# Kernel tuning notes

Measured on AMD Instinct MI355X. Metric: run time of the kernel, lower is better.

The kernel has to match this reference:

```python
import jax, jax.numpy as jnp
import numpy as np

N = 32768          # total nodes
B = 64             # number of graphs (batch.max()+1)
IN_C = 256
OUT_C = 256
NUM_SCALES = 4
NUM_HEADS = 8
BN_EPS = 1e-5


def setup_inputs() -> dict:
    key = jax.random.key(0)
    ks = jax.random.split(key, 10)
    out_s = OUT_C // NUM_SCALES
    x = jax.random.normal(ks[0], (N, IN_C), jnp.float32)
    spectral = jax.random.normal(ks[1], (NUM_SCALES, N, IN_C), jnp.float32)
    batch = jnp.sort(jax.random.randint(ks[2], (N,), 0, B)).astype(jnp.int64)
    # per-scale Linear weights (glorot) and zero biases; stored as [S, in, out_s]
    g = (6.0 / (IN_C + out_s)) ** 0.5
    Ws = jax.random.uniform(ks[3], (NUM_SCALES, IN_C, out_s), jnp.float32, -g, g)
    bs = jnp.zeros((NUM_SCALES, out_s), jnp.float32)
    # MultiheadAttention params (torch layout: in_proj [3E,E], out_proj [E,E])
    s_in = (1.0 / OUT_C) ** 0.5
    W_in = jax.random.uniform(ks[4], (3 * OUT_C, OUT_C), jnp.float32, -s_in, s_in)
    b_in = jnp.zeros((3 * OUT_C,), jnp.float32)
    W_out = jax.random.uniform(ks[5], (OUT_C, OUT_C), jnp.float32, -s_in, s_in)
    b_out = jnp.zeros((OUT_C,), jnp.float32)
    gamma = jnp.ones((OUT_C,), jnp.float32)
    beta = jnp.zeros((OUT_C,), jnp.float32)
    return {"x": x, "spectral": spectral, "Ws": Ws, "bs": bs,
            "W_in": W_in, "b_in": b_in, "W_out": W_out, "b_out": b_out,
            "gamma": gamma, "beta": beta, "batch": batch}


def _forward(x, spectral, Ws, bs, W_in, b_in, W_out, b_out, gamma, beta, batch):
    n, E = x.shape[0], W_out.shape[0]
    # per-scale linear on (x + spectral_feat), concat over scales -> [N, E]
    scale_out = jnp.einsum('sni,sio->sno', x[None] + spectral, Ws) + bs[:, None, :]
    h = jnp.moveaxis(scale_out, 0, 1).reshape(n, E)
    # ragged -> dense padding (batch is sorted segment ids)
    counts = jnp.bincount(batch, length=B)
    max_nodes = int(np.asarray(counts).max())  # data-dependent pad, as in torch
    starts = jnp.concatenate([jnp.zeros((1,), counts.dtype), jnp.cumsum(counts)[:-1]])
    pos = jnp.arange(n) - starts[batch]
    h_pad = jnp.zeros((B, max_nodes, E), h.dtype).at[batch, pos].set(h)
    # MHA over padded graphs (no key-padding mask, matching the source)
    hd = E // NUM_HEADS
    qkv = h_pad @ W_in.T + b_in                       # [B, M, 3E]
    q, k, v = jnp.split(qkv, 3, axis=-1)
    def heads(t):
        return t.reshape(B, max_nodes, NUM_HEADS, hd).transpose(0, 2, 1, 3)
    q, k, v = heads(q) * (hd ** -0.5), heads(k), heads(v)
    attn = jax.nn.softmax(jnp.einsum('bhqd,bhkd->bhqk', q, k), axis=-1)
    ctx = jnp.einsum('bhqk,bhkd->bhqd', attn, v)
    ctx = ctx.transpose(0, 2, 1, 3).reshape(B, max_nodes, E)
    h_att = ctx @ W_out.T + b_out
    # dense -> ragged unpad
    h2 = h_att[batch, pos]                            # [N, E]
    # BatchNorm1d (training-mode batch stats, deterministic) + ReLU; dropout=eval
    mean = h2.mean(axis=0)
    var = h2.var(axis=0)
    hn = (h2 - mean) * jax.lax.rsqrt(var + BN_EPS) * gamma + beta
    return jax.nn.relu(hn)


def reference(x, spectral, Ws, bs, W_in, b_in, W_out, b_out, gamma, beta, batch):
    return _forward(x, spectral, Ws, bs, W_in, b_in, W_out, b_out, gamma, beta, batch)
```

## Files before the change

### kernel.cpp

```cpp
#include <hip/hip_runtime.h>


typedef __attribute__((ext_vector_type(8))) short frag8;
typedef __attribute__((ext_vector_type(4))) short frag4;
typedef __attribute__((ext_vector_type(4))) float f32x4;
typedef __attribute__((ext_vector_type(8))) unsigned short ushort8;
typedef __attribute__((ext_vector_type(2))) unsigned int uint2e;

#define NN 32768
#define NB 64
#define CIN 256
#define COUT 256
#define NHEAD 8
#define HD 32

#define BM 128
#define LDB 264
#define KT 128

#if __has_builtin(__builtin_amdgcn_mfma_f32_16x16x16bf16_1k)
#define HAS_MFMA16 1
#else
#define HAS_MFMA16 0
#endif

#if __has_builtin(__builtin_amdgcn_exp2f)
#define EXP2(x) __builtin_amdgcn_exp2f(x)
#else
#define EXP2(x) __expf((x) * 0.6931471805599453f)
#endif

__device__ inline unsigned short f2bf(float f) {
  unsigned u = __builtin_bit_cast(unsigned, f);
  u += 0x7FFFu + ((u >> 16) & 1u);
  return (unsigned short)(u >> 16);
}
__device__ inline float bf2f(unsigned short h) {
  return __builtin_bit_cast(float, (unsigned)h << 16);
}
__device__ inline unsigned cvtpk(float a, float b) {
  unsigned r;
  asm("v_cvt_pk_bf16_f32 %0, %1, %2" : "=v"(r) : "v"(a), "v"(b));
  return r;
}

__global__ void k_prep(const float* __restrict__ Ws, const float* __restrict__ Win,
                       const float* __restrict__ Wout, const int* __restrict__ batch,
                       unsigned short* __restrict__ wst, unsigned short* __restrict__ winb,
                       unsigned short* __restrict__ woutb, int* __restrict__ meta) {
  int tid = blockIdx.x * 256 + threadIdx.x;
  if (tid < NN) {
    int v = batch[tid];
    int prev = (tid == 0) ? -1 : batch[tid - 1];
    for (int bb = prev + 1; bb <= v; ++bb) meta[NB + bb] = tid;
  }
  if (tid < 4 * 64 * 256) {
    int s = tid >> 14, rem = tid & 16383, o = rem >> 8, i = rem & 255;
    wst[tid] = f2bf(Ws[((s * 256) + i) * 64 + o]);
  } else if (tid < 4 * 64 * 256 + 768 * 256) {
    int t2 = tid - 4 * 64 * 256;
    winb[t2] = f2bf(Win[t2]);
  } else if (tid < 4 * 64 * 256 + 768 * 256 + 256 * 256) {
    int t3 = tid - (4 * 64 * 256 + 768 * 256);
    woutb[t3] = f2bf(Wout[t3]);
  }
}
__global__ void k_meta2(int* __restrict__ meta) {
  __shared__ int mx[NB];
  int b = threadIdx.x;
  int s = meta[NB + b];
  int e = (b == 63) ? NN : meta[NB + b + 1];
  meta[b] = e - s;
  mx[b] = e - s;
  __syncthreads();
  if (b == 0) {
    int m = 0;
    for (int j = 0; j < NB; ++j) m = max(m, mx[j]);
    meta[2 * NB] = m;
  }
}

__device__ inline void stage_Bpanel(const unsigned short* __restrict__ Wt,
                                    unsigned short (*Bs)[LDB], int t) {
  int n = t >> 2, seg = t & 3;
  const unsigned short* src = Wt + (size_t)n * 256 + seg * 64;
#pragma unroll
  for (int i = 0; i < 8; ++i) {
    uint4 v = *(const uint4*)(src + i * 8);
    *(uint4*)&Bs[n][seg * 64 + i * 8] = v;
  }
}


__global__ __launch_bounds__(256, 4) void k_scale(const float* __restrict__ x,
                                                  const float* __restrict__ spec,
                                                  const unsigned short* __restrict__ wst,
                                                  const float* __restrict__ bs,
                                                  unsigned short* __restrict__ h) {
  __shared__ unsigned short Bs[64][LDB];
  int t = threadIdx.x, lane = t & 63, wave = t >> 6;
  int r0 = blockIdx.x * BM, s = blockIdx.y;
  int m16 = lane & 15, quad = lane >> 4;

  stage_Bpanel(wst + (size_t)s * 64 * 256, Bs, t);

  const float* sb = spec + (size_t)s * NN * CIN;
  size_t rowbase0 = (size_t)(r0 + wave * 32 + m16) * CIN + quad * 8;
  size_t rowbase1 = rowbase0 + 16 * CIN;

  float4 P[3][4];
#define ISSUE(slot, kc, mi)                                              \
  do {                                                                   \
    size_t base_ = ((mi) ? rowbase1 : rowbase0) + (size_t)(kc) * 32;     \
    P[(slot)][0] = *(const float4*)(x + base_);                          \
    P[(slot)][1] = *(const float4*)(x + base_ + 4);                      \
    P[(slot)][2] = *(const float4*)(sb + base_);                         \
    P[(slot)][3] = *(const float4*)(sb + base_ + 4);                     \
  } while (0)

  ISSUE(0, 0, 0);
  ISSUE(1, 0, 1);
  ISSUE(2, 1, 0);

  __syncthreads();

  f32x4 z = {0.f, 0.f, 0.f, 0.f};
  f32x4 acc[2][4];
#pragma unroll
  for (int mi = 0; mi < 2; ++mi)
#pragma unroll
    for (int ni = 0; ni < 4; ++ni) acc[mi][ni] = z;

#pragma unroll
  for (int st = 0; st < 16; ++st) {
    const int kc = st >> 1, mi = st & 1, slot = st % 3;
    uint4 u;
    u.x = cvtpk(P[slot][0].x + P[slot][2].x, P[slot][0].y + P[slot][2].y);
    u.y = cvtpk(P[slot][0].z + P[slot][2].z, P[slot][0].w + P[slot][2].w);
    u.z = cvtpk(P[slot][1].x + P[slot][3].x, P[slot][1].y + P[slot][3].y);
    u.w = cvtpk(P[slot][1].z + P[slot][3].z, P[slot][1].w + P[slot][3].w);
    frag8 a = __builtin_bit_cast(frag8, u);
    if (st + 3 < 16) ISSUE(slot, (st + 3) >> 1, (st + 3) & 1);
    frag8 b0 = *(const frag8*)&Bs[m16][kc * 32 + quad * 8];
    frag8 b1 = *(const frag8*)&Bs[16 + m16][kc * 32 + quad * 8];
    frag8 b2 = *(const frag8*)&Bs[32 + m16][kc * 32 + quad * 8];
    frag8 b3 = *(const frag8*)&Bs[48 + m16][kc * 32 + quad * 8];
    acc[mi][0] = __builtin_amdgcn_mfma_f32_16x16x32_bf16(a, b0, acc[mi][0], 0, 0, 0);
    acc[mi][1] = __builtin_amdgcn_mfma_f32_16x16x32_bf16(a, b1, acc[mi][1], 0, 0, 0);
    acc[mi][2] = __builtin_amdgcn_mfma_f32_16x16x32_bf16(a, b2, acc[mi][2], 0, 0, 0);
    acc[mi][3] = __builtin_amdgcn_mfma_f32_16x16x32_bf16(a, b3, acc[mi][3], 0, 0, 0);
  }
#undef ISSUE

#pragma unroll
  for (int mi = 0; mi < 2; ++mi)
#pragma unroll
    for (int ni = 0; ni < 4; ++ni) {
      int col = ni * 16 + m16;
      float bias = bs[s * 64 + col];
#pragma unroll
      for (int rp = 0; rp < 2; ++rp) {
        int row = r0 + wave * 32 + mi * 16 + quad * 4 + rp * 2;
        unsigned u = cvtpk(acc[mi][ni][rp * 2] + bias, acc[mi][ni][rp * 2 + 1] + bias);
        h[(size_t)row * COUT + s * 64 + col] = (unsigned short)u;
        h[(size_t)(row + 1) * COUT + s * 64 + col] = (unsigned short)(u >> 16);
      }
    }
}

template <int LDOUT>
__global__ __launch_bounds__(256, 4) void k_lin(const unsigned short* __restrict__ A,
                                                const unsigned short* __restrict__ Wt,
                                                const float* __restrict__ bias,
                                                unsigned short* __restrict__ out) {
  __shared__ unsigned short Bs[64][LDB];
  int t = threadIdx.x, lane = t & 63, wave = t >> 6;
  int r0 = blockIdx.x * BM, c0 = blockIdx.y * 64;
  int m16 = lane & 15, quad = lane >> 4;

  stage_Bpanel(Wt + (size_t)c0 * 256, Bs, t);

  const unsigned short* pa0 = A + (size_t)(r0 + wave * 32 + m16) * 256 + quad * 8;
  const unsigned short* pa1 = pa0 + 16 * 256;

  frag8 PA[3];
  PA[0] = *(const frag8*)(pa0);
  PA[1] = *(const frag8*)(pa1);
  PA[2] = *(const frag8*)(pa0 + 32);

  __syncthreads();

  f32x4 z = {0.f, 0.f, 0.f, 0.f};
  f32x4 acc[2][4];
#pragma unroll
  for (int mi = 0; mi < 2; ++mi)
#pragma unroll
    for (int ni = 0; ni < 4; ++ni) acc[mi][ni] = z;

#pragma unroll
  for (int st = 0; st < 16; ++st) {
    const int kc = st >> 1, mi = st & 1, slot = st % 3;
    frag8 a = PA[slot];
    if (st + 3 < 16) {
      const int nst = st + 3;
      PA[slot] = *(const frag8*)(((nst & 1) ? pa1 : pa0) + (nst >> 1) * 32);
    }
    frag8 b0 = *(const frag8*)&Bs[m16][kc * 32 + quad * 8];
    frag8 b1 = *(const frag8*)&Bs[16 + m16][kc * 32 + quad * 8];
    frag8 b2 = *(const frag8*)&Bs[32 + m16][kc * 32 + quad * 8];
    frag8 b3 = *(const frag8*)&Bs[48 + m16][kc * 32 + quad * 8];
    acc[mi][0] = __builtin_amdgcn_mfma_f32_16x16x32_bf16(a, b0, acc[mi][0], 0, 0, 0);
    acc[mi][1] = __builtin_amdgcn_mfma_f32_16x16x32_bf16(a, b1, acc[mi][1], 0, 0, 0);
    acc[mi][2] = __builtin_amdgcn_mfma_f32_16x16x32_bf16(a, b2, acc[mi][2], 0, 0, 0);
    acc[mi][3] = __builtin_amdgcn_mfma_f32_16x16x32_bf16(a, b3, acc[mi][3], 0, 0, 0);
  }

#pragma unroll
  for (int mi = 0; mi < 2; ++mi)
#pragma unroll
    for (int ni = 0; ni < 4; ++ni) {
      int col = c0 + ni * 16 + m16;
      float bv = bias[col];
#pragma unroll
      for (int rp = 0; rp < 2; ++rp) {
        int row = r0 + wave * 32 + mi * 16 + quad * 4 + rp * 2;
        unsigned u = cvtpk(acc[mi][ni][rp * 2] + bv, acc[mi][ni][rp * 2 + 1] + bv);
        out[(size_t)row * LDOUT + col] = (unsigned short)u;
        out[(size_t)(row + 1) * LDOUT + col] = (unsigned short)(u >> 16);
      }
    }
}

__global__ __launch_bounds__(256) void k_attn_mfma(const unsigned short* __restrict__ qkv,
                                                   const int* __restrict__ meta,
                                                   unsigned short* __restrict__ ctx) {
  int b = blockIdx.x >> 3, head = blockIdx.x & 7;
  int c = meta[b], st = meta[NB + b], M = meta[2 * NB];

  __shared__ unsigned short Vt[32][KT + 8];

  int t = threadIdx.x, lane = t & 63, wave = t >> 6;
  int m16 = lane & 15, quad = lane >> 4;
  const float SC2 = 0.17677669529663687f * 1.4426950408889634f;
  float extra = (float)(M - c);

#if !HAS_MFMA16
  int sl0 = m16 + ((quad & 1) << 5);
  int sl1 = sl0 + 16;
#endif

  for (int q0 = 0; q0 < c; q0 += 128) {
    int qbase = q0 + wave * 32;
    frag8 qf[2];
#pragma unroll
    for (int qg = 0; qg < 2; ++qg) {
      int qrow = qbase + qg * 16 + m16;
      qf[qg] = *(const frag8*)(qkv + (size_t)(st + qrow) * 768 + head * 32 + quad * 8);
    }

    f32x4 zz = {0.f, 0.f, 0.f, 0.f};
    f32x4 O[2][2];
    float lp[2] = {0.f, 0.f};
#pragma unroll
    for (int qg = 0; qg < 2; ++qg) { O[qg][0] = zz; O[qg][1] = zz; }

    for (int kt = 0; kt < c; kt += KT) {
      {
        int key = t >> 1, dh0 = (t & 1) * 16;
        const unsigned short* vp = qkv + (size_t)(st + kt + key) * 768 + 512 + head * 32 + dh0;
        ushort8 v0 = *(const ushort8*)vp;
        ushort8 v1 = *(const ushort8*)(vp + 8);
#pragma unroll
        for (int i = 0; i < 8; ++i) {
          Vt[dh0 + i][key] = v0[i];
          Vt[dh0 + 8 + i][key] = v1[i];
        }
      }
      __syncthreads();

#pragma unroll
      for (int sub = 0; sub < 4; ++sub) {
        int ks = kt + sub * 32;
        if (ks < c) {
          bool full = (ks + 32 <= c);
          frag8 kf[2];
#pragma unroll
          for (int kh = 0; kh < 2; ++kh) {
            int krow = ks + kh * 16 + m16;
            kf[kh] = *(const frag8*)(qkv + (size_t)(st + krow) * 768 + 256 + head * 32 + quad * 8);
          }
          unsigned pk[2][2][2];
#pragma unroll
          for (int qg = 0; qg < 2; ++qg)
#pragma unroll
            for (int kh = 0; kh < 2; ++kh) {
              f32x4 s = __builtin_amdgcn_mfma_f32_16x16x32_bf16(kf[kh], qf[qg], zz, 0, 0, 0);
              float p[4];
#pragma unroll
              for (int r = 0; r < 4; ++r) p[r] = EXP2(s[r] * SC2);
              if (!full) {
#pragma unroll
                for (int r = 0; r < 4; ++r)
                  if (ks + kh * 16 + quad * 4 + r >= c) p[r] = 0.f;
              }
              lp[qg] += (p[0] + p[1]) + (p[2] + p[3]);
              pk[qg][kh][0] = cvtpk(p[0], p[1]);
              pk[qg][kh][1] = cvtpk(p[2], p[3]);
            }
#if HAS_MFMA16
          frag4 vb[2][2];
#pragma unroll
          for (int kh = 0; kh < 2; ++kh)
#pragma unroll
            for (int dh = 0; dh < 2; ++dh)
              vb[kh][dh] = *(const frag4*)&Vt[dh * 16 + m16][sub * 32 + kh * 16 + quad * 4];
#pragma unroll
          for (int qg = 0; qg < 2; ++qg) {
            frag4 pa0 = __builtin_bit_cast(frag4, uint2e{pk[qg][0][0], pk[qg][0][1]});
            frag4 pa1 = __builtin_bit_cast(frag4, uint2e{pk[qg][1][0], pk[qg][1][1]});
#pragma unroll
            for (int dh = 0; dh < 2; ++dh) {
              O[qg][dh] = __builtin_amdgcn_mfma_f32_16x16x16bf16_1k(pa0, vb[0][dh], O[qg][dh], 0, 0, 0);
              O[qg][dh] = __builtin_amdgcn_mfma_f32_16x16x16bf16_1k(pa1, vb[1][dh], O[qg][dh], 0, 0, 0);
            }
          }
#else
          frag8 vf[2];
#pragma unroll
          for (int dh = 0; dh < 2; ++dh)
            vf[dh] = *(const frag8*)&Vt[dh * 16 + m16][sub * 32 + quad * 8];
#pragma unroll
          for (int qg = 0; qg < 2; ++qg) {
            unsigned a0 = __shfl(pk[qg][0][0], sl0), a1 = __shfl(pk[qg][0][1], sl0);
            unsigned a2 = __shfl(pk[qg][0][0], sl1), a3 = __shfl(pk[qg][0][1], sl1);
            unsigned b0 = __shfl(pk[qg][1][0], sl0), b1 = __shfl(pk[qg][1][1], sl0);
            unsigned b2 = __shfl(pk[qg][1][0], sl1), b3 = __shfl(pk[qg][1][1], sl1);
            uint4 pw;
            pw.x = (quad < 2) ? a0 : b0;
            pw.y = (quad < 2) ? a1 : b1;
            pw.z = (quad < 2) ? a2 : b2;
            pw.w = (quad < 2) ? a3 : b3;
            frag8 pf = __builtin_bit_cast(frag8, pw);
#pragma unroll
            for (int dh = 0; dh < 2; ++dh)
              O[qg][dh] = __builtin_amdgcn_mfma_f32_16x16x32_bf16(pf, vf[dh], O[qg][dh], 0, 0, 0);
          }
#endif
        }
      }
      __syncthreads();
    }

#pragma unroll
    for (int qg = 0; qg < 2; ++qg) {
      float v = lp[qg];
      v += __shfl_xor(v, 16);
      v += __shfl_xor(v, 32);
      lp[qg] = v;
    }

#pragma unroll
    for (int qg = 0; qg < 2; ++qg)
#pragma unroll
      for (int r = 0; r < 4; ++r) {
        int qrow = qbase + qg * 16 + quad * 4 + r;
        float lsum = __shfl(lp[qg], quad * 4 + r);
        if (qrow < c) {
          float inv = 1.f / (lsum + extra);
          unsigned short* op = ctx + (size_t)(st + qrow) * 256 + head * 32;
          unsigned u = cvtpk(O[qg][0][r] * inv, O[qg][1][r] * inv);
          op[m16] = (unsigned short)u;
          op[16 + m16] = (unsigned short)(u >> 16);
        }
      }
  }
}

__global__ __launch_bounds__(256) void k_stats(const unsigned short* __restrict__ h,
                                               float* __restrict__ sums) {
  int c = threadIdx.x;
  int r0 = blockIdx.x * 64;
  float s = 0.f, s2 = 0.f;
#pragma unroll 8
  for (int r = 0; r < 64; ++r) {
    float v = bf2f(h[(size_t)(r0 + r) * 256 + c]);
    s += v; s2 += v * v;
  }
  atomicAdd(&sums[c], s);
  atomicAdd(&sums[256 + c], s2);
}

__global__ __launch_bounds__(256) void k_bn_apply(const unsigned short* __restrict__ h,
                                                  const float* __restrict__ sums,
                                                  const float* __restrict__ gamma,
                                                  const float* __restrict__ beta,
                                                  float* __restrict__ out) {
  size_t i8 = ((size_t)blockIdx.x * 256 + threadIdx.x) * 8;
  int c0 = (int)(i8 & 255);
  ushort8 v = *(const ushort8*)(h + i8);
  float4 o0, o1;
  float res[8];
#pragma unroll
  for (int i = 0; i < 8; ++i) {
    int ch = c0 + i;
    float mean = sums[ch] * (1.0f / NN);
    float var = sums[256 + ch] * (1.0f / NN) - mean * mean;
    float sc = rsqrtf(var + 1e-5f) * gamma[ch];
    float sh = beta[ch] - mean * sc;
    res[i] = fmaxf(bf2f(v[i]) * sc + sh, 0.f);
  }
  o0.x = res[0]; o0.y = res[1]; o0.z = res[2]; o0.w = res[3];
  o1.x = res[4]; o1.y = res[5]; o1.z = res[6]; o1.w = res[7];
  *(float4*)(out + i8) = o0;
  *(float4*)(out + i8 + 4) = o1;
}

extern "C" void kernel_launch(void* const* d_in, const int* in_sizes, int n_in,
                              void* d_out, int out_size, void* d_ws, size_t ws_size,
                              hipStream_t stream) {
  const float* x      = (const float*)d_in[0];
  const float* spec   = (const float*)d_in[1];
  const float* Ws     = (const float*)d_in[2];
  const float* bs     = (const float*)d_in[3];
  const float* Win    = (const float*)d_in[4];
  const float* b_in   = (const float*)d_in[5];
  const float* Wout   = (const float*)d_in[6];
  const float* b_out  = (const float*)d_in[7];
  const float* gamma  = (const float*)d_in[8];
  const float* beta   = (const float*)d_in[9];
  const int* batch    = (const int*)d_in[10];
  float* out = (float*)d_out;

  char* w = (char*)d_ws;
  size_t off = 0;
  auto alloc = [&](size_t bytes) -> void* {
    off = (off + 255) & ~(size_t)255;
    void* p = w + off; off += bytes; return p;
  };
  int* meta             = (int*)alloc(129 * sizeof(int));
  unsigned short* wst   = (unsigned short*)alloc((size_t)4 * 64 * 256 * 2);
  unsigned short* winb  = (unsigned short*)alloc((size_t)768 * 256 * 2);
  unsigned short* woutb = (unsigned short*)alloc((size_t)256 * 256 * 2);
  float* sums           = (float*)alloc(512 * 4);
  unsigned short* h     = (unsigned short*)alloc((size_t)NN * 256 * 2);
  unsigned short* qkv   = (unsigned short*)alloc((size_t)NN * 768 * 2);
  unsigned short* ctx   = (unsigned short*)alloc((size_t)NN * 256 * 2);
  unsigned short* hatt  = (unsigned short*)alloc((size_t)NN * 256 * 2);

  (void)hipMemsetAsync(sums, 0, 512 * 4, stream);
  k_prep<<<1280, 256, 0, stream>>>(Ws, Win, Wout, batch, wst, winb, woutb, meta);
  k_meta2<<<1, 64, 0, stream>>>(meta);
  k_scale<<<dim3(NN / BM, 4), 256, 0, stream>>>(x, spec, wst, bs, h);
  k_lin<768><<<dim3(NN / BM, 12), 256, 0, stream>>>(h, winb, b_in, qkv);
  k_attn_mfma<<<NB * NHEAD, 256, 0, stream>>>(qkv, meta, ctx);
  k_lin<256><<<dim3(NN / BM, 4), 256, 0, stream>>>(ctx, woutb, b_out, hatt);
  k_stats<<<NN / 64, 256, 0, stream>>>(hatt, sums);
  k_bn_apply<<<NN * 256 / 2048, 256, 0, stream>>>(hatt, sums, gamma, beta, out);
}
```

Before: 430.3 us.

## Split attention query tiles across grid and store QKV head-major

The attention kernel now runs one block per (graph, head, 128-query tile), with a second grid dimension of 8, instead of looping over query tiles inside a block. This raises parallelism from 512 blocks to up to 4096. The QKV projection now writes a head-major layout, [24 heads][N][32], so each head's Q/K/V rows are contiguous 64-byte runs. The risk is that K/V are reloaded by every query-tile block, and the strided 2-byte epilogue stores in the projection may coalesce worse. The grid also assumes at most 1024 nodes per graph.

```diff
diff --git a/kernel.cpp b/kernel.cpp
--- a/kernel.cpp
+++ b/kernel.cpp
@@ -168,7 +168,7 @@
     }
 }
 
-template <int LDOUT>
+template <int LDOUT, bool HEADMAJOR>
 __global__ __launch_bounds__(256, 4) void k_lin(const unsigned short* __restrict__ A,
                                                 const unsigned short* __restrict__ Wt,
                                                 const float* __restrict__ bias,
@@ -221,12 +221,21 @@
     for (int ni = 0; ni < 4; ++ni) {
       int col = c0 + ni * 16 + m16;
       float bv = bias[col];
+      unsigned short* ob;
+      size_t rstride;
+      if (HEADMAJOR) {
+        ob = out + (size_t)(col >> 5) * ((size_t)NN * 32) + (col & 31);
+        rstride = 32;
+      } else {
+        ob = out + col;
+        rstride = LDOUT;
+      }
 #pragma unroll
       for (int rp = 0; rp < 2; ++rp) {
         int row = r0 + wave * 32 + mi * 16 + quad * 4 + rp * 2;
         unsigned u = cvtpk(acc[mi][ni][rp * 2] + bv, acc[mi][ni][rp * 2 + 1] + bv);
-        out[(size_t)row * LDOUT + col] = (unsigned short)u;
-        out[(size_t)(row + 1) * LDOUT + col] = (unsigned short)(u >> 16);
+        ob[(size_t)row * rstride] = (unsigned short)u;
+        ob[(size_t)(row + 1) * rstride] = (unsigned short)(u >> 16);
       }
     }
 }
@@ -236,6 +245,12 @@
                                                    unsigned short* __restrict__ ctx) {
   int b = blockIdx.x >> 3, head = blockIdx.x & 7;
   int c = meta[b], st = meta[NB + b], M = meta[2 * NB];
+  int q0 = blockIdx.y * 128;
+  if (q0 >= c) return;
+
+  const unsigned short* Qp = qkv + (size_t)head * ((size_t)NN * 32);
+  const unsigned short* Kp = qkv + (size_t)(8 + head) * ((size_t)NN * 32);
+  const unsigned short* Vp = qkv + (size_t)(16 + head) * ((size_t)NN * 32);
 
   __shared__ unsigned short Vt[32][KT + 8];
 
@@ -244,136 +259,134 @@
   const float SC2 = 0.17677669529663687f * 1.4426950408889634f;
   float extra = (float)(M - c);
 
+  int qbase = q0 + wave * 32;
+  frag8 qf[2];
+#pragma unroll
+  for (int qg = 0; qg < 2; ++qg) {
+    int qrow = qbase + qg * 16 + m16;
+    qf[qg] = *(const frag8*)(Qp + (size_t)(st + qrow) * 32 + quad * 8);
+  }
+
+  f32x4 zz = {0.f, 0.f, 0.f, 0.f};
+  f32x4 O[2][2];
+  float lp[2] = {0.f, 0.f};
+#pragma unroll
+  for (int qg = 0; qg < 2; ++qg) { O[qg][0] = zz; O[qg][1] = zz; }
+
 #if !HAS_MFMA16
   int sl0 = m16 + ((quad & 1) << 5);
   int sl1 = sl0 + 16;
 #endif
 
-  for (int q0 = 0; q0 < c; q0 += 128) {
-    int qbase = q0 + wave * 32;
-    frag8 qf[2];
-#pragma unroll
-    for (int qg = 0; qg < 2; ++qg) {
-      int qrow = qbase + qg * 16 + m16;
-      qf[qg] = *(const frag8*)(qkv + (size_t)(st + qrow) * 768 + head * 32 + quad * 8);
-    }
-
-    f32x4 zz = {0.f, 0.f, 0.f, 0.f};
-    f32x4 O[2][2];
-    float lp[2] = {0.f, 0.f};
-#pragma unroll
-    for (int qg = 0; qg < 2; ++qg) { O[qg][0] = zz; O[qg][1] = zz; }
-
-    for (int kt = 0; kt < c; kt += KT) {
-      {
-        int key = t >> 1, dh0 = (t & 1) * 16;
-        const unsigned short* vp = qkv + (size_t)(st + kt + key) * 768 + 512 + head * 32 + dh0;
-        ushort8 v0 = *(const ushort8*)vp;
-        ushort8 v1 = *(const ushort8*)(vp + 8);
-#pragma unroll
-        for (int i = 0; i < 8; ++i) {
-          Vt[dh0 + i][key] = v0[i];
-          Vt[dh0 + 8 + i][key] = v1[i];
+  for (int kt = 0; kt < c; kt += KT) {
+    {
+      int key = t >> 1, dh0 = (t & 1) * 16;
+      const unsigned short* vp = Vp + (size_t)(st + kt + key) * 32 + dh0;
+      ushort8 v0 = *(const ushort8*)vp;
+      ushort8 v1 = *(const ushort8*)(vp + 8);
+#pragma unroll
+      for (int i = 0; i < 8; ++i) {
+        Vt[dh0 + i][key] = v0[i];
+        Vt[dh0 + 8 + i][key] = v1[i];
+      }
+    }
+    __syncthreads();
+
+#pragma unroll
+    for (int sub = 0; sub < 4; ++sub) {
+      int ks = kt + sub * 32;
+      if (ks < c) {
+        bool full = (ks + 32 <= c);
+        frag8 kf[2];
+#pragma unroll
+        for (int kh = 0; kh < 2; ++kh) {
+          int krow = ks + kh * 16 + m16;
+          kf[kh] = *(const frag8*)(Kp + (size_t)(st + krow) * 32 + quad * 8);
         }
-      }
-      __syncthreads();
-
-#pragma unroll
-      for (int sub = 0; sub < 4; ++sub) {
-        int ks = kt + sub * 32;
-        if (ks < c) {
-          bool full = (ks + 32 <= c);
-          frag8 kf[2];
+        unsigned pk[2][2][2];
+#pragma unroll
+        for (int qg = 0; qg < 2; ++qg)
 #pragma unroll
           for (int kh = 0; kh < 2; ++kh) {
-            int krow = ks + kh * 16 + m16;
-            kf[kh] = *(const frag8*)(qkv + (size_t)(st + krow) * 768 + 256 + head * 32 + quad * 8);
+            f32x4 s = __builtin_amdgcn_mfma_f32_16x16x32_bf16(kf[kh], qf[qg], zz, 0, 0, 0);
+            float p[4];
+#pragma unroll
+            for (int r = 0; r < 4; ++r) p[r] = EXP2(s[r] * SC2);
+            if (!full) {
+#pragma unroll
+              for (int r = 0; r < 4; ++r)
+                if (ks + kh * 16 + quad * 4 + r >= c) p[r] = 0.f;
+            }
+            lp[qg] += (p[0] + p[1]) + (p[2] + p[3]);
+            pk[qg][kh][0] = cvtpk(p[0], p[1]);
+            pk[qg][kh][1] = cvtpk(p[2], p[3]);
           }
-          unsigned pk[2][2][2];
-#pragma unroll
-          for (int qg = 0; qg < 2; ++qg)
-#pragma unroll
-            for (int kh = 0; kh < 2; ++kh) {
-              f32x4 s = __builtin_amdgcn_mfma_f32_16x16x32_bf16(kf[kh], qf[qg], zz, 0, 0, 0);
-              float p[4];
-#pragma unroll
-              for (int r = 0; r < 4; ++r) p[r] = EXP2(s[r] * SC2);
-              if (!full) {
-#pragma unroll
-                for (int r = 0; r < 4; ++r)
-                  if (ks + kh * 16 + quad * 4 + r >= c) p[r] = 0.f;
-              }
-              lp[qg] += (p[0] + p[1]) + (p[2] + p[3]);
-              pk[qg][kh][0] = cvtpk(p[0], p[1]);
-              pk[qg][kh][1] = cvtpk(p[2], p[3]);
-            }
 #if HAS_MFMA16
-          frag4 vb[2][2];
-#pragma unroll
-          for (int kh = 0; kh < 2; ++kh)
-#pragma unroll
-            for (int dh = 0; dh < 2; ++dh)
-              vb[kh][dh] = *(const frag4*)&Vt[dh * 16 + m16][sub * 32 + kh * 16 + quad * 4];
-#pragma unroll
-          for (int qg = 0; qg < 2; ++qg) {
-            frag4 pa0 = __builtin_bit_cast(frag4, uint2e{pk[qg][0][0], pk[qg][0][1]});
-            frag4 pa1 = __builtin_bit_cast(frag4, uint2e{pk[qg][1][0], pk[qg][1][1]});
-#pragma unroll
-            for (int dh = 0; dh < 2; ++dh) {
-              O[qg][dh] = __builtin_amdgcn_mfma_f32_16x16x16bf16_1k(pa0, vb[0][dh], O[qg][dh], 0, 0, 0);
-              O[qg][dh] = __builtin_amdgcn_mfma_f32_16x16x16bf16_1k(pa1, vb[1][dh], O[qg][dh], 0, 0, 0);
-            }
+        frag4 vb[2][2];
+#pragma unroll
+        for (int kh = 0; kh < 2; ++kh)
+#pragma unroll
+          for (int dh = 0; dh < 2; ++dh)
+            vb[kh][dh] = *(const frag4*)&Vt[dh * 16 + m16][sub * 32 + kh * 16 + quad * 4];
+#pragma unroll
+        for (int qg = 0; qg < 2; ++qg) {
+          frag4 pa0 = __builtin_bit_cast(frag4, uint2e{pk[qg][0][0], pk[qg][0][1]});
+          frag4 pa1 = __builtin_bit_cast(frag4, uint2e{pk[qg][1][0], pk[qg][1][1]});
+#pragma unroll
+          for (int dh = 0; dh < 2; ++dh) {
+            O[qg][dh] = __builtin_amdgcn_mfma_f32_16x16x16bf16_1k(pa0, vb[0][dh], O[qg][dh], 0, 0, 0);
+            O[qg][dh] = __builtin_amdgcn_mfma_f32_16x16x16bf16_1k(pa1, vb[1][dh], O[qg][dh], 0, 0, 0);
           }
+        }
 #else
-          frag8 vf[2];
+        frag8 vf[2];
+#pragma unroll
+        for (int dh = 0; dh < 2; ++dh)
+          vf[dh] = *(const frag8*)&Vt[dh * 16 + m16][sub * 32 + quad * 8];
+#pragma unroll
+        for (int qg = 0; qg < 2; ++qg) {
+          unsigned a0 = __shfl(pk[qg][0][0], sl0), a1 = __shfl(pk[qg][0][1], sl0);
+          unsigned a2 = __shfl(pk[qg][0][0], sl1), a3 = __shfl(pk[qg][0][1], sl1);
+          unsigned b0 = __shfl(pk[qg][1][0], sl0), b1 = __shfl(pk[qg][1][1], sl0);
+          unsigned b2 = __shfl(pk[qg][1][0], sl1), b3 = __shfl(pk[qg][1][1], sl1);
+          uint4 pw;
+          pw.x = (quad < 2) ? a0 : b0;
+          pw.y = (quad < 2) ? a1 : b1;
+          pw.z = (quad < 2) ? a2 : b2;
+          pw.w = (quad < 2) ? a3 : b3;
+          frag8 pf = __builtin_bit_cast(frag8, pw);
 #pragma unroll
           for (int dh = 0; dh < 2; ++dh)
-            vf[dh] = *(const frag8*)&Vt[dh * 16 + m16][sub * 32 + quad * 8];
-#pragma unroll
-          for (int qg = 0; qg < 2; ++qg) {
-            unsigned a0 = __shfl(pk[qg][0][0], sl0), a1 = __shfl(pk[qg][0][1], sl0);
-            unsigned a2 = __shfl(pk[qg][0][0], sl1), a3 = __shfl(pk[qg][0][1], sl1);
-            unsigned b0 = __shfl(pk[qg][1][0], sl0), b1 = __shfl(pk[qg][1][1], sl0);
-            unsigned b2 = __shfl(pk[qg][1][0], sl1), b3 = __shfl(pk[qg][1][1], sl1);
-            uint4 pw;
-            pw.x = (quad < 2) ? a0 : b0;
-            pw.y = (quad < 2) ? a1 : b1;
-            pw.z = (quad < 2) ? a2 : b2;
-            pw.w = (quad < 2) ? a3 : b3;
-            frag8 pf = __builtin_bit_cast(frag8, pw);
-#pragma unroll
-            for (int dh = 0; dh < 2; ++dh)
-              O[qg][dh] = __builtin_amdgcn_mfma_f32_16x16x32_bf16(pf, vf[dh], O[qg][dh], 0, 0, 0);
-          }
+            O[qg][dh] = __builtin_amdgcn_mfma_f32_16x16x32_bf16(pf, vf[dh], O[qg][dh], 0, 0, 0);
+        }
 #endif
-        }
-      }
-      __syncthreads();
-    }
-
-#pragma unroll
-    for (int qg = 0; qg < 2; ++qg) {
-      float v = lp[qg];
-      v += __shfl_xor(v, 16);
-      v += __shfl_xor(v, 32);
-      lp[qg] = v;
-    }
-
-#pragma unroll
-    for (int qg = 0; qg < 2; ++qg)
-#pragma unroll
-      for (int r = 0; r < 4; ++r) {
-        int qrow = qbase + qg * 16 + quad * 4 + r;
-        float lsum = __shfl(lp[qg], quad * 4 + r);
-        if (qrow < c) {
-          float inv = 1.f / (lsum + extra);
-          unsigned short* op = ctx + (size_t)(st + qrow) * 256 + head * 32;
-          unsigned u = cvtpk(O[qg][0][r] * inv, O[qg][1][r] * inv);
-          op[m16] = (unsigned short)u;
-          op[16 + m16] = (unsigned short)(u >> 16);
-        }
-      }
-  }
+      }
+    }
+    __syncthreads();
+  }
+
+#pragma unroll
+  for (int qg = 0; qg < 2; ++qg) {
+    float v = lp[qg];
+    v += __shfl_xor(v, 16);
+    v += __shfl_xor(v, 32);
+    lp[qg] = v;
+  }
+
+#pragma unroll
+  for (int qg = 0; qg < 2; ++qg)
+#pragma unroll
+    for (int r = 0; r < 4; ++r) {
+      int qrow = qbase + qg * 16 + quad * 4 + r;
+      float lsum = __shfl(lp[qg], quad * 4 + r);
+      if (qrow < c) {
+        float inv = 1.f / (lsum + extra);
+        unsigned short* op = ctx + (size_t)(st + qrow) * 256 + head * 32;
+        unsigned u = cvtpk(O[qg][0][r] * inv, O[qg][1][r] * inv);
+        op[m16] = (unsigned short)u;
+        op[16 + m16] = (unsigned short)(u >> 16);
+      }
+    }
 }
 
 __global__ __launch_bounds__(256) void k_stats(const unsigned short* __restrict__ h,
@@ -451,9 +464,9 @@
   k_prep<<<1280, 256, 0, stream>>>(Ws, Win, Wout, batch, wst, winb, woutb, meta);
   k_meta2<<<1, 64, 0, stream>>>(meta);
   k_scale<<<dim3(NN / BM, 4), 256, 0, stream>>>(x, spec, wst, bs, h);
-  k_lin<768><<<dim3(NN / BM, 12), 256, 0, stream>>>(h, winb, b_in, qkv);
-  k_attn_mfma<<<NB * NHEAD, 256, 0, stream>>>(qkv, meta, ctx);
-  k_lin<256><<<dim3(NN / BM, 4), 256, 0, stream>>>(ctx, woutb, b_out, hatt);
+  k_lin<768, true><<<dim3(NN / BM, 12), 256, 0, stream>>>(h, winb, b_in, qkv);
+  k_attn_mfma<<<dim3(NB * NHEAD, 8), 256, 0, stream>>>(qkv, meta, ctx);
+  k_lin<256, false><<<dim3(NN / BM, 4), 256, 0, stream>>>(ctx, woutb, b_out, hatt);
   k_stats<<<NN / 64, 256, 0, stream>>>(hatt, sums);
   k_bn_apply<<<NN * 256 / 2048, 256, 0, stream>>>(hatt, sums, gamma, beta, out);
 }
```

Result: faster. 381.5 us (-11.3%).
